# Kernel optimization log

Hardware: AMD Instinct MI355X
Metric: run time of the kernel (lower is better)

## Reference

```python
import jax, jax.numpy as jnp
import numpy as np

FILTER_LENGTH = 2048
HOP_LENGTH = 512
CUTOFF = FILTER_LENGTH // 2 + 1  # 1025


def _make_forward_basis():
    # Real/imag rows of DFT matrix, modulated by periodic Hann window.
    fourier_basis = np.fft.fft(np.eye(FILTER_LENGTH))
    basis = np.vstack([np.real(fourier_basis[:CUTOFF, :]),
                       np.imag(fourier_basis[:CUTOFF, :])])  # [2050, 2048]
    n = np.arange(FILTER_LENGTH)
    hann = 0.5 - 0.5 * np.cos(2.0 * np.pi * n / FILTER_LENGTH)  # fftbins=True
    basis = basis * hann[None, :]
    return jnp.asarray(basis[:, None, :], dtype=jnp.float32)  # [2050, 1, 2048]


def setup_inputs() -> dict:
    key = jax.random.key(0)
    input_data = jax.random.normal(key, (32, 320000), dtype=jnp.float32)
    forward_basis = _make_forward_basis()
    return {"input_data": input_data, "forward_basis": forward_basis}


def reference(input_data, forward_basis):
    B = input_data.shape[0]
    pad = FILTER_LENGTH // 2
    x = jnp.pad(input_data, ((0, 0), (pad, pad)), mode="reflect")  # [B, N+2048]
    x = x[:, None, :]  # [B, 1, T]
    ft = jax.lax.conv_general_dilated(
        x, forward_basis,
        window_strides=(HOP_LENGTH,),
        padding="VALID",
        dimension_numbers=("NCH", "OIH", "NCH"),
    )  # [B, 2050, frames]
    real = ft[:, :CUTOFF, :]
    imag = ft[:, CUTOFF:, :]
    return jnp.sqrt(real * real + imag * imag)
```

## Files before the change

kernel.cpp:

```cpp
#include <hip/hip_runtime.h>
#include <hip/hip_bf16.h>
#include <cstdint>


#define FILT   2048
#define HOP    512
#define CUT    1025
#define NBATCH 32
#define TFR    626
#define NFR    (NBATCH * TFR)
#define LSIG   320000
#define LPAD   (LSIG + FILT)
#define N2     1024

typedef __attribute__((ext_vector_type(8))) short short8;

__device__ __forceinline__ short bf16r(float f) {
  __hip_bfloat16 h = __float2bfloat16(f);
  return __builtin_bit_cast(short, h);
}
__device__ __forceinline__ float bf2f(uint32_t u) {
  return __builtin_bit_cast(float, u << 16);
}

__device__ __forceinline__ short8 pack8(float4 a, float4 b) {
  short8 v;
  v[0] = bf16r(a.x); v[1] = bf16r(a.y); v[2] = bf16r(a.z); v[3] = bf16r(a.w);
  v[4] = bf16r(b.x); v[5] = bf16r(b.y); v[6] = bf16r(b.z); v[7] = bf16r(b.w);
  return v;
}

__global__ void pad_signal(const float* __restrict__ x, short* __restrict__ XP) {
  const int b = blockIdx.y;
  const int i0 = (blockIdx.x * 256 + threadIdx.x) * 8;
  if (i0 >= LPAD) return;
  const float* xb = x + (size_t)b * LSIG;
  const int j0 = i0 - 1024;
  short8 v;
  if (j0 >= 0 && j0 + 8 <= LSIG) {
    float4 a = *(const float4*)(xb + j0);
    float4 c = *(const float4*)(xb + j0 + 4);
    v = pack8(a, c);
  } else {
    #pragma unroll
    for (int e = 0; e < 8; ++e) {
      int j = j0 + e;
      j = j < 0 ? -j : (j >= LSIG ? 2 * LSIG - 2 - j : j);
      v[e] = bf16r(xb[j]);
    }
  }
  *(short8*)&XP[(size_t)b * LPAD + i0] = v;
}

__global__ void make_tables(float* __restrict__ hann, float2* __restrict__ Tst,
                            float2* __restrict__ Tun) {
  const int i = blockIdx.x * 256 + threadIdx.x;
  const float PI2 = 6.283185307179586f;
  if (i < 2048) hann[i] = 0.5f - 0.5f * cosf(PI2 * (float)i / 2048.0f);
  if (i < 1024) {
    float s, c;
    sincosf(-PI2 * (float)i / 1024.0f, &s, &c);
    Tst[i] = make_float2(c, s);
    sincosf(-PI2 * (float)i / 2048.0f, &s, &c);
    Tun[i] = make_float2(c, s);
  }
}

__device__ __forceinline__ float2 cmul(float2 a, float2 b) {
  return make_float2(a.x * b.x - a.y * b.y, a.x * b.y + a.y * b.x);
}
__device__ __forceinline__ float2 cmulc(float2 a, float cx, float cy) {
  return make_float2(a.x * cx - a.y * cy, a.x * cy + a.y * cx);
}

__device__ __forceinline__ int SW(int i) { return i ^ ((i >> 4) & 15); }

__device__ __forceinline__ void fft16(float2* y) {
  static constexpr float TX[4][4] = {
    {1.f, 1.f, 1.f, 1.f},
    {1.f,  0.92387953251128674f,  0.70710678118654752f,  0.38268343236508978f},
    {1.f,  0.70710678118654752f,  0.f,                  -0.70710678118654752f},
    {1.f,  0.38268343236508978f, -0.70710678118654752f, -0.92387953251128674f}};
  static constexpr float TY[4][4] = {
    {0.f, 0.f, 0.f, 0.f},
    {0.f, -0.38268343236508978f, -0.70710678118654752f, -0.92387953251128674f},
    {0.f, -0.70710678118654752f, -1.f,                  -0.70710678118654752f},
    {0.f, -0.92387953251128674f, -0.70710678118654752f,  0.38268343236508978f}};
  float2 G[16];
  #pragma unroll
  for (int n0 = 0; n0 < 4; ++n0) {
    float2 a0 = y[n0], a1 = y[n0 + 4], a2 = y[n0 + 8], a3 = y[n0 + 12];
    float2 e = make_float2(a0.x + a2.x, a0.y + a2.y);
    float2 f = make_float2(a0.x - a2.x, a0.y - a2.y);
    float2 g = make_float2(a1.x + a3.x, a1.y + a3.y);
    float2 h = make_float2(a1.x - a3.x, a1.y - a3.y);
    float2 F0 = make_float2(e.x + g.x, e.y + g.y);
    float2 F1 = make_float2(f.x + h.y, f.y - h.x);
    float2 F2 = make_float2(e.x - g.x, e.y - g.y);
    float2 F3 = make_float2(f.x - h.y, f.y + h.x);
    G[n0 * 4 + 0] = F0;
    G[n0 * 4 + 1] = cmulc(F1, TX[n0][1], TY[n0][1]);
    G[n0 * 4 + 2] = cmulc(F2, TX[n0][2], TY[n0][2]);
    G[n0 * 4 + 3] = cmulc(F3, TX[n0][3], TY[n0][3]);
  }
  #pragma unroll
  for (int q = 0; q < 4; ++q) {
    float2 a0 = G[q], a1 = G[4 + q], a2 = G[8 + q], a3 = G[12 + q];
    float2 e = make_float2(a0.x + a2.x, a0.y + a2.y);
    float2 f = make_float2(a0.x - a2.x, a0.y - a2.y);
    float2 g = make_float2(a1.x + a3.x, a1.y + a3.y);
    float2 h = make_float2(a1.x - a3.x, a1.y - a3.y);
    y[q]      = make_float2(e.x + g.x, e.y + g.y);
    y[q + 4]  = make_float2(f.x + h.y, f.y - h.x);
    y[q + 8]  = make_float2(e.x - g.x, e.y - g.y);
    y[q + 12] = make_float2(f.x - h.y, f.y + h.x);
  }
}

template<int LOG>
__device__ __forceinline__ void fft_stage(float2* z, const float2* tw, int lane) {
  constexpr int M4 = 1 << LOG;
  constexpr int STRIDE = 1 << (8 - LOG);
  #pragma unroll
  for (int u = 0; u < 4; ++u) {
    const int bf = u * 64 + lane;
    const int j  = bf & (M4 - 1);
    const int i0 = ((bf >> LOG) << (LOG + 2)) | j;
    const int i1 = i0 + M4, i2 = i0 + 2 * M4, i3 = i0 + 3 * M4;
    const int p0 = SW(i0), p1 = SW(i1), p2 = SW(i2), p3 = SW(i3);
    float2 a = z[p0], b = z[p1], c = z[p2], d = z[p3];
    if (LOG > 0) {
      b = cmul(b, tw[j * STRIDE]);
      c = cmul(c, tw[2 * j * STRIDE]);
      d = cmul(d, tw[3 * j * STRIDE]);
    }
    const float2 t0 = make_float2(a.x + c.x, a.y + c.y);
    const float2 t1 = make_float2(a.x - c.x, a.y - c.y);
    const float2 t2 = make_float2(b.x + d.x, b.y + d.y);
    const float2 t3 = make_float2(b.x - d.x, b.y - d.y);
    z[p0] = make_float2(t0.x + t2.x, t0.y + t2.y);
    z[p1] = make_float2(t1.x + t3.y, t1.y - t3.x);
    z[p2] = make_float2(t0.x - t2.x, t0.y - t2.y);
    z[p3] = make_float2(t1.x - t3.y, t1.y + t3.x);
  }
}

__global__ __launch_bounds__(256)
void stft_fft(const short* __restrict__ XP, const float* __restrict__ hann,
              const float2* __restrict__ Tst, const float2* __restrict__ Tun,
              float* __restrict__ out)
{
  __shared__ float2 zsh[4][1024];
  __shared__ float2 tst[1024];
  __shared__ ushort mag[16][1032];

  const int tid = threadIdx.x, wv = tid >> 6, lane = tid & 63;
  #pragma unroll
  for (int u = 0; u < 4; ++u) tst[u * 256 + tid] = Tst[u * 256 + tid];
  __syncthreads();

  float2* z = zsh[wv];
  const int bid = blockIdx.x;

  const int G  = ((lane & 3) << 4) | (lane & 12) | (lane >> 4);
  const int zb = 16 * G, gm = G & 15;

  for (int q = 0; q < 4; ++q) {
    const int f = bid * 16 + q * 4 + wv;
    const int b = f / TFR, t = f - b * TFR;
    const short* base = XP + (size_t)b * LPAD + (size_t)t * HOP;

    float2 y[16];
    #pragma unroll
    for (int u = 0; u < 16; ++u) {
      const int n = u * 64 + lane;
      const uint32_t pr = *(const uint32_t*)(base + 2 * n);
      const float2 h = *(const float2*)(hann + 2 * n);
      y[u] = make_float2(bf2f(pr & 0xffffu) * h.x, bf2f(pr >> 16) * h.y);
    }
    fft16(y);
    #pragma unroll
    for (int k = 0; k < 16; ++k) z[zb + (k ^ gm)] = y[k];

    fft_stage<4>(z, tst, lane);
    fft_stage<6>(z, tst, lane);
    fft_stage<8>(z, tst, lane);

    ushort* mrow = mag[q * 4 + wv];
    #pragma unroll
    for (int v = 0; v < 8; ++v) {
      const int k = v * 64 + lane;
      const float2 Zk = z[SW(k)];
      const int km = (N2 - k) & (N2 - 1);
      const float2 Zm = z[SW(km)];
      const float xer = 0.5f * (Zk.x + Zm.x);
      const float xei = 0.5f * (Zk.y - Zm.y);
      const float xor_ = 0.5f * (Zk.y + Zm.y);
      const float xoi = -0.5f * (Zk.x - Zm.x);
      const float2 w = Tun[k];
      const float px = w.x * xor_ - w.y * xoi;
      const float py = w.x * xoi + w.y * xor_;
      const float Xr = xer + px, Xi = xei + py;
      const float Yr = xer - px, Yi = xei - py;
      mrow[k]        = (ushort)bf16r(sqrtf(Xr * Xr + Xi * Xi));
      mrow[1024 - k] = (ushort)bf16r(sqrtf(Yr * Yr + Yi * Yi));
    }
    if (lane == 0) {
      const float2 Zc = z[SW(512)];
      mrow[512] = (ushort)bf16r(sqrtf(Zc.x * Zc.x + Zc.y * Zc.y));
    }
  }
  __syncthreads();

  const int fq0 = bid * 16;
  const int b0 = fq0 / TFR, t0 = fq0 - b0 * TFR;
  if (t0 + 15 < TFR) {
    for (int kk = tid; kk < 1025; kk += 256) {
      float* p = out + (size_t)b0 * (CUT * TFR) + (size_t)kk * TFR + t0;
      #pragma unroll
      for (int w2 = 0; w2 < 8; ++w2)
        *(float2*)(p + 2 * w2) =
            make_float2(bf2f(mag[2 * w2][kk]), bf2f(mag[2 * w2 + 1][kk]));
    }
  } else {
    for (int kk = tid; kk < 1025; kk += 256) {
      #pragma unroll
      for (int w2 = 0; w2 < 16; ++w2) {
        const int ff = fq0 + w2;
        const int bb = ff / TFR, tt = ff - bb * TFR;
        out[(size_t)bb * (CUT * TFR) + (size_t)kk * TFR + tt] = bf2f(mag[w2][kk]);
      }
    }
  }
}

typedef __attribute__((ext_vector_type(4))) float f32x4;

__global__ __launch_bounds__(256, 2)
void stft_gemm_fb(const float* __restrict__ basis, const float* __restrict__ x,
                  float* __restrict__ out)
{
  __shared__ alignas(16) short sA[2][128][64];
  __shared__ alignas(16) short sB[128][64];

  const int tid  = threadIdx.x;
  const int wave = tid >> 6;
  const int lane = tid & 63;
  const int n0 = blockIdx.x * 128;
  const int m0 = blockIdx.y * 128;

  f32x4 acc_r[4][4], acc_i[4][4];
  #pragma unroll
  for (int i = 0; i < 4; ++i)
    #pragma unroll
    for (int j = 0; j < 4; ++j) { acc_r[i][j] = (f32x4)0.f; acc_i[i][j] = (f32x4)0.f; }

  const int sr = tid >> 1;
  const int sh = (tid & 1) * 32;

  for (int k0 = 0; k0 < FILT; k0 += 64) {
    #pragma unroll
    for (int p = 0; p < 2; ++p) {
      const int k = m0 + sr;
      short8 v[4];
      if (k < CUT) {
        const float* src = basis + (size_t)(p * CUT + k) * FILT + k0 + sh;
        #pragma unroll
        for (int qq = 0; qq < 4; ++qq) {
          float4 a = *(const float4*)(src + qq * 8);
          float4 b = *(const float4*)(src + qq * 8 + 4);
          v[qq] = pack8(a, b);
        }
      } else {
        #pragma unroll
        for (int qq = 0; qq < 4; ++qq) v[qq] = (short8)(short)0;
      }
      #pragma unroll
      for (int qq = 0; qq < 4; ++qq) *(short8*)&sA[p][sr][sh + qq * 8] = v[qq];
    }
    {
      const int f = n0 + sr;
      short8 v[4];
      if (f < NFR) {
        const int b = f / TFR, t = f - b * TFR;
        const float* xb = x + (size_t)b * LSIG;
        const int j0 = t * HOP + k0 + sh - 1024;
        if (j0 >= 0 && j0 + 32 <= LSIG) {
          #pragma unroll
          for (int qq = 0; qq < 4; ++qq) {
            float4 a  = *(const float4*)(xb + j0 + qq * 8);
            float4 b2 = *(const float4*)(xb + j0 + qq * 8 + 4);
            v[qq] = pack8(a, b2);
          }
        } else {
          #pragma unroll
          for (int qq = 0; qq < 4; ++qq)
            #pragma unroll
            for (int e = 0; e < 8; ++e) {
              int j = j0 + qq * 8 + e;
              j = j < 0 ? -j : (j >= LSIG ? 2 * LSIG - 2 - j : j);
              v[qq][e] = bf16r(xb[j]);
            }
        }
      } else {
        #pragma unroll
        for (int qq = 0; qq < 4; ++qq) v[qq] = (short8)(short)0;
      }
      #pragma unroll
      for (int qq = 0; qq < 4; ++qq) *(short8*)&sB[sr][sh + qq * 8] = v[qq];
    }
    __syncthreads();

    const int ra = lane & 15;
    #pragma unroll
    for (int kk = 0; kk < 64; kk += 32) {
      const int col = kk + (lane >> 4) * 8;
      short8 arr[4], aii[4], bfr[4];
      #pragma unroll
      for (int i = 0; i < 4; ++i) {
        const int rm = (wave >> 1) * 64 + i * 16 + ra;
        arr[i] = *(const short8*)&sA[0][rm][col];
        aii[i] = *(const short8*)&sA[1][rm][col];
        const int rn = (wave & 1) * 64 + i * 16 + ra;
        bfr[i] = *(const short8*)&sB[rn][col];
      }
      #pragma unroll
      for (int i = 0; i < 4; ++i)
        #pragma unroll
        for (int j = 0; j < 4; ++j) {
          acc_r[i][j] = __builtin_amdgcn_mfma_f32_16x16x32_bf16(arr[i], bfr[j], acc_r[i][j], 0, 0, 0);
          acc_i[i][j] = __builtin_amdgcn_mfma_f32_16x16x32_bf16(aii[i], bfr[j], acc_i[i][j], 0, 0, 0);
        }
    }
    __syncthreads();
  }

  const int wm0 = m0 + (wave >> 1) * 64;
  const int wn0 = n0 + (wave & 1) * 64;
  const int cl = lane & 15;
  const int rg = (lane >> 4) * 4;
  #pragma unroll
  for (int j = 0; j < 4; ++j) {
    const int f = wn0 + j * 16 + cl;
    if (f >= NFR) continue;
    const int b = f / TFR, t = f - b * TFR;
    float* ob = out + (size_t)b * (CUT * TFR) + t;
    #pragma unroll
    for (int i = 0; i < 4; ++i) {
      #pragma unroll
      for (int r = 0; r < 4; ++r) {
        const int k = wm0 + i * 16 + rg + r;
        if (k < CUT) {
          float re = acc_r[i][j][r], im = acc_i[i][j][r];
          ob[(size_t)k * TFR] = sqrtf(re * re + im * im);
        }
      }
    }
  }
}

extern "C" void kernel_launch(void* const* d_in, const int* in_sizes, int n_in,
                              void* d_out, int out_size, void* d_ws, size_t ws_size,
                              hipStream_t stream) {
  const float* x     = (const float*)d_in[0];
  const float* basis = (const float*)d_in[1];
  float* out = (float*)d_out;

  const size_t sbytes = (size_t)NBATCH * LPAD * sizeof(short);
  const size_t hbytes = 2048 * sizeof(float);
  const size_t tbytes = 1024 * sizeof(float2);

  if (ws_size >= sbytes + hbytes + 2 * tbytes) {
    short*  XP   = (short*)d_ws;
    float*  hann = (float*)((char*)d_ws + sbytes);
    float2* Tst  = (float2*)((char*)d_ws + sbytes + hbytes);
    float2* Tun  = (float2*)((char*)d_ws + sbytes + hbytes + tbytes);
    pad_signal<<<dim3((LPAD + 2047) / 2048, NBATCH), 256, 0, stream>>>(x, XP);
    make_tables<<<8, 256, 0, stream>>>(hann, Tst, Tun);
    stft_fft<<<NFR / 16, 256, 0, stream>>>(XP, hann, Tst, Tun, out);
  } else {
    stft_gemm_fb<<<dim3(157, 9), 256, 0, stream>>>(basis, x, out);
  }
}
```

Measured before the change: 103.3 us.

## Split FFT and output transpose into separate kernels via bf16 workspace

The FFT kernel now computes one frame per wave with a single pass per block and writes bf16 magnitudes frame-major to a global workspace, no longer staging 16 frames in shared memory. A new tiled transpose kernel reads that workspace and writes the frequency-major float output with float4 stores over 32-frame tiles. The aim is higher occupancy in the FFT kernel (less LDS, more blocks) and more coalesced output writes. In exchange it adds an extra global round trip of about 44 MB, a kernel launch, and a larger workspace requirement that could push execution onto the fallback GEMM path if the workspace is too small.

```diff
diff --git a/kernel.cpp b/kernel.cpp
--- a/kernel.cpp
+++ b/kernel.cpp
@@ -12,6 +12,9 @@
 #define LSIG   320000
 #define LPAD   (LSIG + FILT)
 #define N2     1024
+#define MWS    1088
+#define KT     17
+#define TT     20
 
 typedef __attribute__((ext_vector_type(8))) short short8;
 
@@ -148,11 +151,10 @@
 __global__ __launch_bounds__(256)
 void stft_fft(const short* __restrict__ XP, const float* __restrict__ hann,
               const float2* __restrict__ Tst, const float2* __restrict__ Tun,
-              float* __restrict__ out)
+              ushort* __restrict__ MW)
 {
   __shared__ float2 zsh[4][1024];
   __shared__ float2 tst[1024];
-  __shared__ ushort mag[16][1032];
 
   const int tid = threadIdx.x, wv = tid >> 6, lane = tid & 63;
   #pragma unroll
@@ -160,75 +162,93 @@
   __syncthreads();
 
   float2* z = zsh[wv];
-  const int bid = blockIdx.x;
 
   const int G  = ((lane & 3) << 4) | (lane & 12) | (lane >> 4);
   const int zb = 16 * G, gm = G & 15;
 
-  for (int q = 0; q < 4; ++q) {
-    const int f = bid * 16 + q * 4 + wv;
-    const int b = f / TFR, t = f - b * TFR;
-    const short* base = XP + (size_t)b * LPAD + (size_t)t * HOP;
-
-    float2 y[16];
-    #pragma unroll
-    for (int u = 0; u < 16; ++u) {
-      const int n = u * 64 + lane;
-      const uint32_t pr = *(const uint32_t*)(base + 2 * n);
-      const float2 h = *(const float2*)(hann + 2 * n);
-      y[u] = make_float2(bf2f(pr & 0xffffu) * h.x, bf2f(pr >> 16) * h.y);
-    }
-    fft16(y);
-    #pragma unroll
-    for (int k = 0; k < 16; ++k) z[zb + (k ^ gm)] = y[k];
-
-    fft_stage<4>(z, tst, lane);
-    fft_stage<6>(z, tst, lane);
-    fft_stage<8>(z, tst, lane);
-
-    ushort* mrow = mag[q * 4 + wv];
-    #pragma unroll
-    for (int v = 0; v < 8; ++v) {
-      const int k = v * 64 + lane;
-      const float2 Zk = z[SW(k)];
-      const int km = (N2 - k) & (N2 - 1);
-      const float2 Zm = z[SW(km)];
-      const float xer = 0.5f * (Zk.x + Zm.x);
-      const float xei = 0.5f * (Zk.y - Zm.y);
-      const float xor_ = 0.5f * (Zk.y + Zm.y);
-      const float xoi = -0.5f * (Zk.x - Zm.x);
-      const float2 w = Tun[k];
-      const float px = w.x * xor_ - w.y * xoi;
-      const float py = w.x * xoi + w.y * xor_;
-      const float Xr = xer + px, Xi = xei + py;
-      const float Yr = xer - px, Yi = xei - py;
-      mrow[k]        = (ushort)bf16r(sqrtf(Xr * Xr + Xi * Xi));
-      mrow[1024 - k] = (ushort)bf16r(sqrtf(Yr * Yr + Yi * Yi));
-    }
-    if (lane == 0) {
-      const float2 Zc = z[SW(512)];
-      mrow[512] = (ushort)bf16r(sqrtf(Zc.x * Zc.x + Zc.y * Zc.y));
+  const int f = blockIdx.x * 4 + wv;
+  const int b = f / TFR, t = f - b * TFR;
+  const short* base = XP + (size_t)b * LPAD + (size_t)t * HOP;
+
+  float2 y[16];
+  #pragma unroll
+  for (int u = 0; u < 16; ++u) {
+    const int n = u * 64 + lane;
+    const uint32_t pr = *(const uint32_t*)(base + 2 * n);
+    const float2 h = *(const float2*)(hann + 2 * n);
+    y[u] = make_float2(bf2f(pr & 0xffffu) * h.x, bf2f(pr >> 16) * h.y);
+  }
+  fft16(y);
+  #pragma unroll
+  for (int k = 0; k < 16; ++k) z[zb + (k ^ gm)] = y[k];
+
+  fft_stage<4>(z, tst, lane);
+  fft_stage<6>(z, tst, lane);
+  fft_stage<8>(z, tst, lane);
+
+  ushort* mw = MW + (size_t)f * MWS;
+  #pragma unroll
+  for (int v = 0; v < 8; ++v) {
+    const int k = v * 64 + lane;
+    const float2 Zk = z[SW(k)];
+    const int km = (N2 - k) & (N2 - 1);
+    const float2 Zm = z[SW(km)];
+    const float xer = 0.5f * (Zk.x + Zm.x);
+    const float xei = 0.5f * (Zk.y - Zm.y);
+    const float xor_ = 0.5f * (Zk.y + Zm.y);
+    const float xoi = -0.5f * (Zk.x - Zm.x);
+    const float2 w = Tun[k];
+    const float px = w.x * xor_ - w.y * xoi;
+    const float py = w.x * xoi + w.y * xor_;
+    const float Xr = xer + px, Xi = xei + py;
+    const float Yr = xer - px, Yi = xei - py;
+    mw[k]        = (ushort)bf16r(sqrtf(Xr * Xr + Xi * Xi));
+    mw[1024 - k] = (ushort)bf16r(sqrtf(Yr * Yr + Yi * Yi));
+  }
+  if (lane == 0) {
+    const float2 Zc = z[SW(512)];
+    mw[512] = (ushort)bf16r(sqrtf(Zc.x * Zc.x + Zc.y * Zc.y));
+  }
+}
+
+__global__ __launch_bounds__(256)
+void transpose_out(const ushort* __restrict__ MW, float* __restrict__ out) {
+  __shared__ float tile[64][33];
+  const int b  = blockIdx.y;
+  const int kt = blockIdx.x % KT;
+  const int tt = blockIdx.x / KT;
+  const int k0 = kt * 64, t0 = tt * 32;
+  const int tid = threadIdx.x;
+  const int r = tid >> 5, c = tid & 31;
+
+  #pragma unroll
+  for (int s = 0; s < 4; ++s) {
+    const int t = t0 + r + 8 * s;
+    if (t < TFR) {
+      const uint32_t pr =
+        *(const uint32_t*)(MW + (size_t)(b * TFR + t) * MWS + k0 + 2 * c);
+      tile[2 * c][r + 8 * s]     = bf2f(pr & 0xffffu);
+      tile[2 * c + 1][r + 8 * s] = bf2f(pr >> 16);
     }
   }
   __syncthreads();
 
-  const int fq0 = bid * 16;
-  const int b0 = fq0 / TFR, t0 = fq0 - b0 * TFR;
-  if (t0 + 15 < TFR) {
-    for (int kk = tid; kk < 1025; kk += 256) {
-      float* p = out + (size_t)b0 * (CUT * TFR) + (size_t)kk * TFR + t0;
-      #pragma unroll
-      for (int w2 = 0; w2 < 8; ++w2)
-        *(float2*)(p + 2 * w2) =
-            make_float2(bf2f(mag[2 * w2][kk]), bf2f(mag[2 * w2 + 1][kk]));
-    }
-  } else {
-    for (int kk = tid; kk < 1025; kk += 256) {
-      #pragma unroll
-      for (int w2 = 0; w2 < 16; ++w2) {
-        const int ff = fq0 + w2;
-        const int bb = ff / TFR, tt = ff - bb * TFR;
-        out[(size_t)bb * (CUT * TFR) + (size_t)kk * TFR + tt] = bf2f(mag[w2][kk]);
+  const int kk = tid >> 2, toff = (tid & 3) * 8;
+  const int k = k0 + kk;
+  if (k < CUT) {
+    float* pptr = out + (size_t)b * (CUT * TFR) + (size_t)k * TFR + t0 + toff;
+    if (t0 + 32 <= TFR) {
+      float4 v0 = make_float4(tile[kk][toff], tile[kk][toff + 1],
+                              tile[kk][toff + 2], tile[kk][toff + 3]);
+      float4 v1 = make_float4(tile[kk][toff + 4], tile[kk][toff + 5],
+                              tile[kk][toff + 6], tile[kk][toff + 7]);
+      *(float4*)pptr = v0;
+      *(float4*)(pptr + 4) = v1;
+    } else {
+      #pragma unroll
+      for (int e = 0; e < 8; ++e) {
+        const int t = t0 + toff + e;
+        if (t < TFR) pptr[e] = tile[kk][toff + e];
       }
     }
   }
@@ -369,15 +389,18 @@
   const size_t sbytes = (size_t)NBATCH * LPAD * sizeof(short);
   const size_t hbytes = 2048 * sizeof(float);
   const size_t tbytes = 1024 * sizeof(float2);
-
-  if (ws_size >= sbytes + hbytes + 2 * tbytes) {
+  const size_t mbytes = (size_t)NFR * MWS * sizeof(ushort);
+
+  if (ws_size >= sbytes + hbytes + 2 * tbytes + mbytes) {
     short*  XP   = (short*)d_ws;
     float*  hann = (float*)((char*)d_ws + sbytes);
     float2* Tst  = (float2*)((char*)d_ws + sbytes + hbytes);
     float2* Tun  = (float2*)((char*)d_ws + sbytes + hbytes + tbytes);
+    ushort* MW   = (ushort*)((char*)d_ws + sbytes + hbytes + 2 * tbytes);
     pad_signal<<<dim3((LPAD + 2047) / 2048, NBATCH), 256, 0, stream>>>(x, XP);
     make_tables<<<8, 256, 0, stream>>>(hann, Tst, Tun);
-    stft_fft<<<NFR / 16, 256, 0, stream>>>(XP, hann, Tst, Tun, out);
+    stft_fft<<<NFR / 4, 256, 0, stream>>>(XP, hann, Tst, Tun, MW);
+    transpose_out<<<dim3(KT * TT, NBATCH), 256, 0, stream>>>(MW, out);
   } else {
     stft_gemm_fb<<<dim3(157, 9), 256, 0, stream>>>(basis, x, out);
   }
```

Measured after the change: 96.39 us. -6.7%, faster.
